# Kernel tuning notes

Measured on AMD Instinct MI355X. Metric: run time of the kernel, lower is better.

Reference implementation:

```python
import jax, jax.numpy as jnp
import numpy as np

B, S, D_IN, D_OUT = 4, 4096, 1024, 64

def setup_inputs() -> dict:
    key = jax.random.key(0)
    ks = jax.random.split(key, 7)
    return {
        "x":  jax.random.normal(ks[0], (B, S, D_IN), dtype=jnp.float32),
        "Wq": jax.random.normal(ks[1], (D_IN, D_OUT), dtype=jnp.float32) * 0.02,
        "bq": jax.random.normal(ks[2], (D_OUT,), dtype=jnp.float32) * 0.02,
        "Wk": jax.random.normal(ks[3], (D_IN, D_OUT), dtype=jnp.float32) * 0.02,
        "bk": jax.random.normal(ks[4], (D_OUT,), dtype=jnp.float32) * 0.02,
        "Wv": jax.random.normal(ks[5], (D_IN, D_OUT), dtype=jnp.float32) * 0.02,
        "bv": jax.random.normal(ks[6], (D_OUT,), dtype=jnp.float32) * 0.02,
    }

def reference(x, Wq, bq, Wk, bk, Wv, bv):
    # x: [B, S, d_in]
    seq = x.shape[1]
    q = x @ Wq + bq            # [B, S, d_out]
    k = x @ Wk + bk
    v = x @ Wv + bv
    scores = jnp.einsum("bqd,bkd->bqk", q, k)          # [B, S, S]
    causal = jnp.triu(jnp.ones((seq, seq), dtype=bool), k=1)
    scores = jnp.where(causal[None, :, :], -jnp.inf, scores)
    # NOTE: original code scales by sqrt(token_len), not sqrt(d_out) (d_k = keys.shape[1])
    scale = jnp.sqrt(jnp.asarray(seq, dtype=scores.dtype))
    attn = jax.nn.softmax(scores / scale, axis=-1)      # [B, S, S]
    # dropout in the original is applied but its result is discarded -> no-op
    return jnp.einsum("bqk,bkd->bqd", attn, v)          # [B, S, d_out]
```

## Files before the change

### kernel.cpp

```cpp
#include <hip/hip_runtime.h>
#include <math.h>

#define B 4
#define S 4096
#define DIN 1024
#define DOUT 64
#define BS (B * S)

typedef __bf16 bf16;
typedef __bf16 bf16x4 __attribute__((ext_vector_type(4)));
typedef __bf16 bf16x8 __attribute__((ext_vector_type(8)));
typedef float f32x4 __attribute__((ext_vector_type(4)));

#define QSCALE 0.022542110013890053f

#define QS_OFF 0
#define KF_OFF (2u * 1024 * 1024)
#define VF_OFF (4u * 1024 * 1024)
#define WP_OFF (6u * 1024 * 1024)
#define OP_OFF (7u * 1024 * 1024)
#define LP_OFF (23u * 1024 * 1024)

__global__ __launch_bounds__(256) void wpack_kernel(
    const float* __restrict__ Wq, const float* __restrict__ Wk,
    const float* __restrict__ Wv, bf16* __restrict__ wp) {
  const int t = blockIdx.x * 256 + threadIdx.x;
  const int m = t >> 16;
  const int r = t & 65535;
  const int k = r >> 6;
  const int n64 = r & 63;
  const float* W = (m == 0) ? Wq : (m == 1) ? Wk : Wv;
  const float v = W[r];
  const int n = m * 64 + n64;
  const int nt = n >> 4;
  const int lane = ((k >> 3) & 3) * 16 + (n & 15);
  const int idx = ((nt * 32 + (k >> 5)) * 64 + lane) * 8 + (k & 7);
  wp[idx] = (bf16)v;
}

__global__ __launch_bounds__(256, 6) void qkv_mfma_kernel(
    const float* __restrict__ x, const float* __restrict__ bq,
    const float* __restrict__ bk, const float* __restrict__ bv,
    const bf16* __restrict__ wp, bf16* __restrict__ Qs,
    bf16* __restrict__ KF, bf16* __restrict__ VF) {
  __shared__ __align__(16) bf16 xt[2][32][136];

  const int tid = threadIdx.x;
  const int wid = tid >> 6;
  const int lane = tid & 63;
  const int l15 = lane & 15;
  const int quad = lane >> 4;
  const int sel = blockIdx.x % 3;
  const int blk = blockIdx.x / 3;
  const int nt = sel * 4 + wid;

  const int srow = tid >> 3;
  const int sc4 = tid & 7;
  const float* xrow = x + (size_t)(blk * 32 + srow) * DIN + sc4 * 4;
  const bf16x8* wp8 = (const bf16x8*)wp;

  f32x4 acc[2] = {(f32x4)(0.f), (f32x4)(0.f)};

  {
    float4 pf[4];
#pragma unroll
    for (int i = 0; i < 4; ++i) pf[i] = *(const float4*)(xrow + i * 32);
#pragma unroll
    for (int i = 0; i < 4; ++i) {
      bf16x4 c;
      c[0] = (bf16)pf[i].x; c[1] = (bf16)pf[i].y;
      c[2] = (bf16)pf[i].z; c[3] = (bf16)pf[i].w;
      *(bf16x4*)&xt[0][srow][i * 32 + sc4 * 4] = c;
    }
  }
  __syncthreads();

  for (int p = 0; p < 8; ++p) {
    const int buf = p & 1;
    float4 pf[4];
    if (p < 7) {
#pragma unroll
      for (int i = 0; i < 4; ++i)
        pf[i] = *(const float4*)(xrow + (p + 1) * 128 + i * 32);
    }
#pragma unroll
    for (int i = 0; i < 4; ++i) {
      const int kc = p * 4 + i;
      const bf16x8 bfr = wp8[(nt * 32 + kc) * 64 + lane];
      const bf16x8 a0 = *(const bf16x8*)&xt[buf][l15][i * 32 + quad * 8];
      const bf16x8 a1 = *(const bf16x8*)&xt[buf][16 + l15][i * 32 + quad * 8];
      acc[0] = __builtin_amdgcn_mfma_f32_16x16x32_bf16(a0, bfr, acc[0], 0, 0, 0);
      acc[1] = __builtin_amdgcn_mfma_f32_16x16x32_bf16(a1, bfr, acc[1], 0, 0, 0);
    }
    if (p < 7) {
      __syncthreads();
#pragma unroll
      for (int i = 0; i < 4; ++i) {
        bf16x4 c;
        c[0] = (bf16)pf[i].x; c[1] = (bf16)pf[i].y;
        c[2] = (bf16)pf[i].z; c[3] = (bf16)pf[i].w;
        *(bf16x4*)&xt[buf ^ 1][srow][i * 32 + sc4 * 4] = c;
      }
      __syncthreads();
    }
  }

  const int c = wid * 16 + l15;
  const float bias = ((sel == 0) ? bq : (sel == 1) ? bk : bv)[c];
#pragma unroll
  for (int st = 0; st < 2; ++st) {
    const int row0 = blk * 32 + st * 16 + quad * 4;
    if (sel == 0) {
#pragma unroll
      for (int r = 0; r < 4; ++r)
        Qs[(size_t)(row0 + r) * DOUT + c] =
            (bf16)((acc[st][r] + bias) * QSCALE);
    } else if (sel == 1) {
      const size_t kb =
          ((size_t)(((row0 >> 6) * 4 + ((row0 >> 4) & 3)) * 2 + (c >> 5)) * 64 +
           ((c >> 3) & 3) * 16 + quad * 4) * 8 + (c & 7);
#pragma unroll
      for (int r = 0; r < 4; ++r)
        KF[kb + r * 8] = (bf16)(acc[st][r] + bias);
    } else {
      const size_t vb =
          ((size_t)(((row0 >> 6) * 2 + ((row0 >> 5) & 1)) * 4 + (c >> 4)) * 64 +
           (c & 15) + 16 * ((row0 >> 3) & 3)) * 8 + (row0 & 7);
      bf16x4 vv;
#pragma unroll
      for (int r = 0; r < 4; ++r) vv[r] = (bf16)(acc[st][r] + bias);
      *(bf16x4*)(VF + vb) = vv;
    }
  }
}

__global__ __launch_bounds__(256, 3) void attn_mfma_kernel(
    const bf16* __restrict__ Qs, const bf16* __restrict__ KFp,
    const bf16* __restrict__ VFp, bf16* __restrict__ Oh,
    float* __restrict__ lh) {
  __shared__ __align__(16) bf16 pw[4][32][72];

  const int tid = threadIdx.x;
  const int wid = tid >> 6;
  const int lane = tid & 63;
  const int l15 = lane & 15;
  const int quad = lane >> 4;
  const int b = blockIdx.x & 3;
  const int half = (blockIdx.x >> 2) & 1;
  const int s32 = 127 - (blockIdx.x >> 3);
  const int ntiles = (s32 >> 1) + 1;
  const int e = half * 4 + wid;
  const int t0 = (e * ntiles) >> 3;
  const int t1 = ((e + 1) * ntiles) >> 3;

  const bf16x8* KF8 = (const bf16x8*)KFp;
  const bf16x8* VF8 = (const bf16x8*)VFp;
  const int tb0 = b * 64;

  const bf16* Qb = Qs + ((size_t)b * S + s32 * 32) * DOUT;
  bf16x8 qf[2][2];
#pragma unroll
  for (int st = 0; st < 2; ++st)
#pragma unroll
    for (int k = 0; k < 2; ++k)
      qf[st][k] =
          *(const bf16x8*)(Qb + (st * 16 + l15) * DOUT + k * 32 + quad * 8);

  f32x4 o[2][4];
#pragma unroll
  for (int st = 0; st < 2; ++st)
#pragma unroll
    for (int i = 0; i < 4; ++i) o[st][i] = (f32x4)(0.f);
  f32x4 lsum[2] = {(f32x4)(0.f), (f32x4)(0.f)};

  bf16x8 kf[8];
  if (t0 < t1) {
    const int tb = tb0 + t0;
#pragma unroll
    for (int nt = 0; nt < 4; ++nt)
#pragma unroll
      for (int c = 0; c < 2; ++c)
        kf[nt * 2 + c] = KF8[(size_t)((tb * 4 + nt) * 2 + c) * 64 + lane];
  }

  for (int t = t0; t < t1; ++t) {
    const int tb = tb0 + t;
    bf16x8 vf[8];
#pragma unroll
    for (int c = 0; c < 2; ++c)
#pragma unroll
      for (int ntd = 0; ntd < 4; ++ntd)
        vf[c * 4 + ntd] = VF8[(size_t)((tb * 2 + c) * 4 + ntd) * 64 + lane];

    const int klim = (t == ntiles - 1) ? 0 : (1 << 24);
#pragma unroll
    for (int nt = 0; nt < 4; ++nt) {
      f32x4 s0 = __builtin_amdgcn_mfma_f32_16x16x32_bf16(
          qf[0][0], kf[nt * 2 + 0], (f32x4)(0.f), 0, 0, 0);
      s0 = __builtin_amdgcn_mfma_f32_16x16x32_bf16(qf[0][1], kf[nt * 2 + 1],
                                                   s0, 0, 0, 0);
      f32x4 s1 = __builtin_amdgcn_mfma_f32_16x16x32_bf16(
          qf[1][0], kf[nt * 2 + 0], (f32x4)(0.f), 0, 0, 0);
      s1 = __builtin_amdgcn_mfma_f32_16x16x32_bf16(qf[1][1], kf[nt * 2 + 1],
                                                   s1, 0, 0, 0);
      const int key = t * 64 + nt * 16 + l15;
#pragma unroll
      for (int r = 0; r < 4; ++r) {
        const int q0 = s32 * 32 + quad * 4 + r + klim;
        const float p0 = (key <= q0) ? exp2f(fminf(s0[r], 44.f)) : 0.f;
        lsum[0][r] += p0;
        pw[wid][quad * 4 + r][nt * 16 + l15] = (bf16)p0;
        const float p1 = (key <= q0 + 16) ? exp2f(fminf(s1[r], 44.f)) : 0.f;
        lsum[1][r] += p1;
        pw[wid][16 + quad * 4 + r][nt * 16 + l15] = (bf16)p1;
      }
    }

    if (t + 1 < t1) {
      const int tbn = tb + 1;
#pragma unroll
      for (int nt = 0; nt < 4; ++nt)
#pragma unroll
        for (int c = 0; c < 2; ++c)
          kf[nt * 2 + c] = KF8[(size_t)((tbn * 4 + nt) * 2 + c) * 64 + lane];
    }

#pragma unroll
    for (int st = 0; st < 2; ++st) {
      const bf16x8 pf0 = *(const bf16x8*)&pw[wid][st * 16 + l15][quad * 8];
      const bf16x8 pf1 = *(const bf16x8*)&pw[wid][st * 16 + l15][32 + quad * 8];
#pragma unroll
      for (int ntd = 0; ntd < 4; ++ntd) {
        o[st][ntd] = __builtin_amdgcn_mfma_f32_16x16x32_bf16(
            pf0, vf[0 * 4 + ntd], o[st][ntd], 0, 0, 0);
        o[st][ntd] = __builtin_amdgcn_mfma_f32_16x16x32_bf16(
            pf1, vf[1 * 4 + ntd], o[st][ntd], 0, 0, 0);
      }
    }
  }

#pragma unroll
  for (int m = 1; m < 16; m <<= 1)
#pragma unroll
    for (int st = 0; st < 2; ++st)
#pragma unroll
      for (int r = 0; r < 4; ++r) lsum[st][r] += __shfl_xor(lsum[st][r], m, 64);

  const int slot = (b * 128 + s32) * 8 + e;
  if (l15 == 0) {
#pragma unroll
    for (int st = 0; st < 2; ++st)
#pragma unroll
      for (int r = 0; r < 4; ++r)
        lh[slot * 32 + st * 16 + quad * 4 + r] = lsum[st][r];
  }
#pragma unroll
  for (int st = 0; st < 2; ++st)
#pragma unroll
    for (int ntd = 0; ntd < 4; ++ntd)
#pragma unroll
      for (int r = 0; r < 4; ++r)
        Oh[(size_t)slot * 2048 + (st * 16 + quad * 4 + r) * 64 + ntd * 16 + l15] =
            (bf16)o[st][ntd][r];
}

__global__ __launch_bounds__(256) void combine_kernel(
    const bf16* __restrict__ Oh, const float* __restrict__ lh,
    float* __restrict__ out) {
  const int gid = blockIdx.x * 256 + threadIdx.x;
  const int token = gid >> 4;
  const int d4 = (gid & 15) * 4;
  const int b = token >> 12;
  const int s = token & 4095;
  const int s32 = s >> 5;
  const int qq = s & 31;
  const int slot0 = (b * 128 + s32) * 8;
  f32x4 acc = (f32x4)(0.f);
  float l = 0.f;
#pragma unroll
  for (int q = 0; q < 8; ++q) {
    const bf16x4 ov =
        *(const bf16x4*)(Oh + (size_t)(slot0 + q) * 2048 + qq * 64 + d4);
#pragma unroll
    for (int i = 0; i < 4; ++i) acc[i] += (float)ov[i];
    l += lh[(slot0 + q) * 32 + qq];
  }
  ((f32x4*)out)[gid] = acc * (1.f / l);
}

extern "C" void kernel_launch(void* const* d_in, const int* in_sizes, int n_in,
                              void* d_out, int out_size, void* d_ws,
                              size_t ws_size, hipStream_t stream) {
  const float* x  = (const float*)d_in[0];
  const float* Wq = (const float*)d_in[1];
  const float* bq = (const float*)d_in[2];
  const float* Wk = (const float*)d_in[3];
  const float* bk = (const float*)d_in[4];
  const float* Wv = (const float*)d_in[5];
  const float* bv = (const float*)d_in[6];
  float* out = (float*)d_out;

  char* ws = (char*)d_ws;
  bf16* Qs = (bf16*)(ws + QS_OFF);
  bf16* KF = (bf16*)(ws + KF_OFF);
  bf16* VF = (bf16*)(ws + VF_OFF);
  bf16* wp = (bf16*)(ws + WP_OFF);
  bf16* Oh = (bf16*)(ws + OP_OFF);
  float* lh = (float*)(ws + LP_OFF);

  wpack_kernel<<<768, 256, 0, stream>>>(Wq, Wk, Wv, wp);
  qkv_mfma_kernel<<<1536, 256, 0, stream>>>(x, bq, bk, bv, wp, Qs, KF, VF);
  attn_mfma_kernel<<<1024, 256, 0, stream>>>(Qs, KF, VF, Oh, lh);
  combine_kernel<<<1024, 256, 0, stream>>>(Oh, lh, out);
}
```

Before: 155.3 us.

## Compute Q, K and V in one block so x is read once

Restructures the QKV projection so each block handles 16 rows and produces all three projections, with each wave computing three 16-column tiles. Previously each block produced only one of Q/K/V for 32 rows, so the fp32 input was streamed from memory three times. The trade-off is more weight fragment loads per MFMA, fewer rows per block, and lower occupancy bounds.

```diff
diff --git a/kernel.cpp b/kernel.cpp
--- a/kernel.cpp
+++ b/kernel.cpp
@@ -38,97 +38,103 @@
   wp[idx] = (bf16)v;
 }
 
-__global__ __launch_bounds__(256, 6) void qkv_mfma_kernel(
+__global__ __launch_bounds__(256, 4) void qkv_mfma_kernel(
     const float* __restrict__ x, const float* __restrict__ bq,
     const float* __restrict__ bk, const float* __restrict__ bv,
     const bf16* __restrict__ wp, bf16* __restrict__ Qs,
     bf16* __restrict__ KF, bf16* __restrict__ VF) {
-  __shared__ __align__(16) bf16 xt[2][32][136];
+  __shared__ __align__(16) bf16 xt[2][16][264];
 
   const int tid = threadIdx.x;
   const int wid = tid >> 6;
   const int lane = tid & 63;
   const int l15 = lane & 15;
   const int quad = lane >> 4;
-  const int sel = blockIdx.x % 3;
-  const int blk = blockIdx.x / 3;
-  const int nt = sel * 4 + wid;
-
-  const int srow = tid >> 3;
-  const int sc4 = tid & 7;
-  const float* xrow = x + (size_t)(blk * 32 + srow) * DIN + sc4 * 4;
+  const int blk = blockIdx.x;
+
   const bf16x8* wp8 = (const bf16x8*)wp;
 
-  f32x4 acc[2] = {(f32x4)(0.f), (f32x4)(0.f)};
+  f32x4 acc[3];
+#pragma unroll
+  for (int j = 0; j < 3; ++j) acc[j] = (f32x4)(0.f);
+
+  const float* xb = x + (size_t)blk * 16 * DIN;
 
   {
-    float4 pf[4];
-#pragma unroll
-    for (int i = 0; i < 4; ++i) pf[i] = *(const float4*)(xrow + i * 32);
+    float4 v[4];
+#pragma unroll
+    for (int i = 0; i < 4; ++i)
+      v[i] = *(const float4*)(xb + (size_t)(i * 4 + wid) * DIN + lane * 4);
 #pragma unroll
     for (int i = 0; i < 4; ++i) {
       bf16x4 c;
-      c[0] = (bf16)pf[i].x; c[1] = (bf16)pf[i].y;
-      c[2] = (bf16)pf[i].z; c[3] = (bf16)pf[i].w;
-      *(bf16x4*)&xt[0][srow][i * 32 + sc4 * 4] = c;
+      c[0] = (bf16)v[i].x; c[1] = (bf16)v[i].y;
+      c[2] = (bf16)v[i].z; c[3] = (bf16)v[i].w;
+      *(bf16x4*)&xt[0][i * 4 + wid][lane * 4] = c;
     }
   }
   __syncthreads();
 
-  for (int p = 0; p < 8; ++p) {
+  for (int p = 0; p < 4; ++p) {
     const int buf = p & 1;
-    float4 pf[4];
-    if (p < 7) {
+    float4 v[4];
+    if (p < 3) {
 #pragma unroll
       for (int i = 0; i < 4; ++i)
-        pf[i] = *(const float4*)(xrow + (p + 1) * 128 + i * 32);
-    }
-#pragma unroll
-    for (int i = 0; i < 4; ++i) {
-      const int kc = p * 4 + i;
-      const bf16x8 bfr = wp8[(nt * 32 + kc) * 64 + lane];
-      const bf16x8 a0 = *(const bf16x8*)&xt[buf][l15][i * 32 + quad * 8];
-      const bf16x8 a1 = *(const bf16x8*)&xt[buf][16 + l15][i * 32 + quad * 8];
-      acc[0] = __builtin_amdgcn_mfma_f32_16x16x32_bf16(a0, bfr, acc[0], 0, 0, 0);
-      acc[1] = __builtin_amdgcn_mfma_f32_16x16x32_bf16(a1, bfr, acc[1], 0, 0, 0);
-    }
-    if (p < 7) {
+        v[i] = *(const float4*)(xb + (size_t)(i * 4 + wid) * DIN +
+                                (p + 1) * 256 + lane * 4);
+    }
+#pragma unroll
+    for (int i = 0; i < 8; ++i) {
+      const int kc = p * 8 + i;
+      bf16x8 bfr[3];
+#pragma unroll
+      for (int j = 0; j < 3; ++j)
+        bfr[j] = wp8[((wid * 3 + j) * 32 + kc) * 64 + lane];
+      const bf16x8 a = *(const bf16x8*)&xt[buf][l15][i * 32 + quad * 8];
+#pragma unroll
+      for (int j = 0; j < 3; ++j)
+        acc[j] = __builtin_amdgcn_mfma_f32_16x16x32_bf16(a, bfr[j], acc[j], 0, 0, 0);
+    }
+    if (p < 3) {
       __syncthreads();
 #pragma unroll
       for (int i = 0; i < 4; ++i) {
         bf16x4 c;
-        c[0] = (bf16)pf[i].x; c[1] = (bf16)pf[i].y;
-        c[2] = (bf16)pf[i].z; c[3] = (bf16)pf[i].w;
-        *(bf16x4*)&xt[buf ^ 1][srow][i * 32 + sc4 * 4] = c;
+        c[0] = (bf16)v[i].x; c[1] = (bf16)v[i].y;
+        c[2] = (bf16)v[i].z; c[3] = (bf16)v[i].w;
+        *(bf16x4*)&xt[buf ^ 1][i * 4 + wid][lane * 4] = c;
       }
       __syncthreads();
     }
   }
 
-  const int c = wid * 16 + l15;
-  const float bias = ((sel == 0) ? bq : (sel == 1) ? bk : bv)[c];
-#pragma unroll
-  for (int st = 0; st < 2; ++st) {
-    const int row0 = blk * 32 + st * 16 + quad * 4;
+#pragma unroll
+  for (int j = 0; j < 3; ++j) {
+    const int nt = wid * 3 + j;
+    const int sel = nt >> 2;
+    const int c = (nt & 3) * 16 + l15;
+    const float bias = ((sel == 0) ? bq : (sel == 1) ? bk : bv)[c];
+    const int row0 = blk * 16 + quad * 4;
     if (sel == 0) {
 #pragma unroll
       for (int r = 0; r < 4; ++r)
         Qs[(size_t)(row0 + r) * DOUT + c] =
-            (bf16)((acc[st][r] + bias) * QSCALE);
+            (bf16)((acc[j][r] + bias) * QSCALE);
     } else if (sel == 1) {
       const size_t kb =
           ((size_t)(((row0 >> 6) * 4 + ((row0 >> 4) & 3)) * 2 + (c >> 5)) * 64 +
            ((c >> 3) & 3) * 16 + quad * 4) * 8 + (c & 7);
 #pragma unroll
       for (int r = 0; r < 4; ++r)
-        KF[kb + r * 8] = (bf16)(acc[st][r] + bias);
+        KF[kb + r * 8] = (bf16)(acc[j][r] + bias);
     } else {
       const size_t vb =
           ((size_t)(((row0 >> 6) * 2 + ((row0 >> 5) & 1)) * 4 + (c >> 4)) * 64 +
            (c & 15) + 16 * ((row0 >> 3) & 3)) * 8 + (row0 & 7);
       bf16x4 vv;
 #pragma unroll
-      for (int r = 0; r < 4; ++r) vv[r] = (bf16)(acc[st][r] + bias);
+      for (int r = 0; r < 4; ++r) vv[r] = (bf16)(acc[j][r] + bias);
       *(bf16x4*)(VF + vb) = vv;
     }
   }
@@ -309,7 +315,7 @@
   float* lh = (float*)(ws + LP_OFF);
 
   wpack_kernel<<<768, 256, 0, stream>>>(Wq, Wk, Wv, wp);
-  qkv_mfma_kernel<<<1536, 256, 0, stream>>>(x, bq, bk, bv, wp, Qs, KF, VF);
+  qkv_mfma_kernel<<<1024, 256, 0, stream>>>(x, bq, bk, bv, wp, Qs, KF, VF);
   attn_mfma_kernel<<<1024, 256, 0, stream>>>(Qs, KF, VF, Oh, lh);
   combine_kernel<<<1024, 256, 0, stream>>>(Oh, lh, out);
 }
```

New measurement: 151.6 us. -2.4%, faster.
